# Kernel optimization log

Measured on AMD Instinct MI355X. Metric: run time of the kernel, lower is better.

The kernel has to match this reference:

```python
import jax, jax.numpy as jnp
import numpy as np

N = 10000      # miRNA_numbers (nodes)
E = 320000     # similarity-graph edges (avg degree 32)
M = 4          # modalities / channel_num (doc, role, tpcp, ernie)
D = 256        # per-modality feature dim (doc_dim=role_dim=tpcp_dim=ernie_dim)
P = 256        # pro_dim
NEG_SLOPE = 0.2  # PyG GATConv default negative_slope


def setup_inputs() -> dict:
    key = jax.random.key(0)
    ks = jax.random.split(key, 10)
    s = 1.0 / np.sqrt(D).astype(np.float32)
    return {
        "x_feats": jax.random.normal(ks[0], (M, N, D), jnp.float32),
        "edge_index": jax.random.randint(ks[1], (2, E), 0, N, dtype=jnp.int32),
        "Wg": jax.random.normal(ks[2], (M, D, D), jnp.float32) * s,      # GAT lin weights
        "a_src": jax.random.normal(ks[3], (M, D), jnp.float32) * s,      # GAT att_src
        "a_dst": jax.random.normal(ks[4], (M, D), jnp.float32) * s,      # GAT att_dst
        "bg": jnp.zeros((M, D), jnp.float32),                            # GAT bias
        "Wp": jax.random.normal(ks[5], (M, D, P), jnp.float32) * s,      # per-modality Linear(d, pro_dim)
        "bp": jnp.zeros((M, P), jnp.float32),
        "conv_w": jax.random.normal(ks[6], (M,), jnp.float32) * 0.5,     # 1x1 Conv2d channel mixer
        "conv_b": jnp.zeros((), jnp.float32),
    }


def reference(x_feats, edge_index, Wg, a_src, a_dst, bg, Wp, bp, conv_w, conv_b):
    n = x_feats.shape[1]
    loop = jnp.arange(n, dtype=edge_index.dtype)
    # PyG GATConv adds self-loops by default
    src = jnp.concatenate([edge_index[0], loop])  # [E+N]
    dst = jnp.concatenate([edge_index[1], loop])  # [E+N]

    def gat(x, W, asrc, adst, b):
        h = x @ W                                            # [N, D]
        alpha = (h * asrc).sum(-1)[src] + (h * adst).sum(-1)[dst]
        alpha = jax.nn.leaky_relu(alpha, NEG_SLOPE)          # [E+N]
        mx = jax.ops.segment_max(alpha, dst, num_segments=n)
        e = jnp.exp(alpha - mx[dst])
        denom = jax.ops.segment_sum(e, dst, num_segments=n) + 1e-16
        coef = e / denom[dst]                                # edge softmax per destination
        out = jax.ops.segment_sum(h[src] * coef[:, None], dst, num_segments=n)
        return out + b

    # 4 modality GATs over the same graph (eval mode: dropout = identity)
    h = jax.nn.relu(jax.vmap(gat)(x_feats, Wg, a_src, a_dst, bg))      # [M, N, D]
    xp = jnp.einsum('mnd,mdp->mnp', h, Wp) + bp[:, None, :]            # per-modality projection
    # 1x1 conv channel fusion across the M modality channels
    fused = jnp.einsum('m,mnp->np', conv_w, xp) + conv_b               # [N, P]
    return fused
```

## Files before the change

kernel.cpp:

```cpp
#include <hip/hip_runtime.h>
#include <hip/hip_bf16.h>
#include <cstdint>
#include <cstddef>

constexpr int kN = 10000;
constexpr int kE = 320000;
constexpr int kM = 4;
constexpr int kD = 256;
constexpr int kP = 256;
constexpr float kSlope = 0.2f;
constexpr int kCap = 96;

typedef __attribute__((ext_vector_type(8))) short bf16x8;
typedef __attribute__((ext_vector_type(4))) float f32x4;
typedef __attribute__((ext_vector_type(2))) float f32x2;

__device__ __forceinline__ unsigned short f2bf(float f) {
  union { float ff; unsigned int i; } v; v.ff = f;
  unsigned int x = v.i;
  unsigned int r = x + 0x7fffu + ((x >> 16) & 1u);
  return (unsigned short)(r >> 16);
}
__device__ __forceinline__ uint4 pack8(float4 a, float4 b) {
  uint4 o;
  o.x = (unsigned)f2bf(a.x) | ((unsigned)f2bf(a.y) << 16);
  o.y = (unsigned)f2bf(a.z) | ((unsigned)f2bf(a.w) << 16);
  o.z = (unsigned)f2bf(b.x) | ((unsigned)f2bf(b.y) << 16);
  o.w = (unsigned)f2bf(b.z) | ((unsigned)f2bf(b.w) << 16);
  return o;
}
__device__ __forceinline__ void gload_lds16(const void* g, void* l) {
  __builtin_amdgcn_global_load_lds((const __attribute__((address_space(1))) unsigned int*)g,
                                   (__attribute__((address_space(3))) unsigned int*)l, 16, 0, 0);
}


__global__ __launch_bounds__(256) void weight_prep_kernel(
    const float* __restrict__ Wg, const float* __restrict__ bp,
    const float* __restrict__ cw, const float* __restrict__ cb,
    unsigned short* __restrict__ Wgt, float* __restrict__ biasp, int* __restrict__ cnt) {
  const int blk = blockIdx.x;
  if (blk >= 65) {
    int z = blk - 65;
    int t = threadIdx.x;
    if (t < 250) ((int4*)cnt)[z * 250 + t] = make_int4(0, 0, 0, 0);
    return;
  }
  if (blk == 64) {
    int p = threadIdx.x;
    float v = cb[0];
#pragma unroll
    for (int mm = 0; mm < kM; mm++) v += cw[mm] * bp[mm * kP + p];
    biasp[p] = v;
    return;
  }
  __shared__ float tile[64][65];
  const int m = blk >> 4;
  const int t2 = blk & 15;
  const int r0 = (t2 >> 2) * 64;
  const int c0 = (t2 & 3) * 64;
  const float* in = Wg + ((size_t)m << 16);
#pragma unroll
  for (int l = 0; l < 16; l++) {
    int idx = l * 256 + threadIdx.x;
    int rr = idx >> 6, cc = idx & 63;
    tile[rr][cc] = in[(size_t)(c0 + rr) * 256 + r0 + cc];
  }
  __syncthreads();
#pragma unroll
  for (int l = 0; l < 16; l++) {
    int idx = l * 256 + threadIdx.x;
    int rr = idx >> 6, cc = idx & 63;
    Wgt[((size_t)m << 16) + (size_t)(r0 + rr) * 256 + c0 + cc] = f2bf(tile[cc][rr]);
  }
}


constexpr int ASTR = 64 * 8 + 8;
constexpr int BSTR = 256 * 8 + 8;
constexpr int kAsBytes = 2 * 4 * ASTR * 2;
constexpr int kBsBytes = 2 * 4 * BSTR * 2;

__global__ __launch_bounds__(256) void gemm_h_csr_mfma(
    const float* __restrict__ x, const unsigned short* __restrict__ Wgt,
    const float* __restrict__ asrc, const float* __restrict__ adst,
    const int* __restrict__ ei, int* __restrict__ cnt, int* __restrict__ csr_src,
    const float* __restrict__ Wp, const float* __restrict__ cw,
    unsigned short* __restrict__ Wqt,
    unsigned short* __restrict__ hb, float* __restrict__ sv, float* __restrict__ tv) {
  const int blk = blockIdx.x;
  const int tid = threadIdx.x;

  __shared__ __align__(16) char smem[kAsBytes + kBsBytes];
  __shared__ float sred[256], tred[256];
  auto As = (unsigned short(*)[4 * ASTR])smem;
  auto Bs = (unsigned short(*)[4 * BSTR])(smem + kAsBytes);

  if (blk >= 945) {
    auto tile = (float(*)[65])smem;
    const int b = blk - 945;
    const int m = b >> 4;
    const int t2 = b & 15;
    const int r0 = (t2 >> 2) * 64;
    const int c0 = (t2 & 3) * 64;
    const float* in = Wp + ((size_t)m << 16);
    const float scale = cw[m];
#pragma unroll
    for (int l = 0; l < 16; l++) {
      int idx = l * 256 + tid;
      int rr = idx >> 6, cc = idx & 63;
      tile[rr][cc] = in[(size_t)(c0 + rr) * 256 + r0 + cc] * scale;
    }
    __syncthreads();
#pragma unroll
    for (int l = 0; l < 16; l++) {
      int idx = l * 256 + tid;
      int rr = idx >> 6, cc = idx & 63;
      Wqt[(size_t)(r0 + rr) * 1024 + (m << 8) + c0 + cc] = f2bf(tile[cc][rr]);
    }
    return;
  }

  if (blk >= 632) {
    int t = (blk - 632) * 256 + tid;
    int e4 = t * 4;
    if (e4 >= kE) return;
    int4 s4 = *(const int4*)&ei[e4];
    int4 d4 = *(const int4*)&ei[kE + e4];
    int sl;
    sl = atomicAdd(&cnt[d4.x], 1); csr_src[d4.x * kCap + sl] = s4.x;
    sl = atomicAdd(&cnt[d4.y], 1); csr_src[d4.y * kCap + sl] = s4.y;
    sl = atomicAdd(&cnt[d4.z], 1); csr_src[d4.z * kCap + sl] = s4.z;
    sl = atomicAdd(&cnt[d4.w], 1); csr_src[d4.w * kCap + sl] = s4.w;
    return;
  }

  const int m = (blk & 7) >> 1;
  const int i = (blk >> 3) * 2 + (blk & 1);
  if (i >= 157) return;
  const int row0 = i * 64;

  const int wave = tid >> 6, lane = tid & 63;
  const int lidx = lane & 15, lslot = lane >> 4;
  const int wcol0 = wave * 64;

  const int arow_s = tid & 63, aslot_s = tid >> 6;
  const int agr = min(row0 + arow_s, kN - 1);
  const float* Abase = x + ((size_t)m * kN + agr) * kD + aslot_s * 8;
  const unsigned short* Bbase = Wgt + (size_t)m * kD * kD;

  f32x4 acc[4][4] = {};

  {
    float4 f0 = *(const float4*)(Abase);
    float4 f1 = *(const float4*)(Abase + 4);
    *(uint4*)&As[0][aslot_s * ASTR + arow_s * 8] = pack8(f0, f1);
#pragma unroll
    for (int l = 0; l < 4; l++) {
      int c = tid + l * 256;
      int col = c & 255, slot = c >> 8;
      gload_lds16(Bbase + (size_t)col * kD + slot * 8, &Bs[0][slot * BSTR + col * 8]);
    }
  }
  __syncthreads();

  int buf = 0;
  for (int t = 0; t < 8; t++) {
    float4 f0, f1;
    const bool pf = (t < 7);
    if (pf) {
      const int k1 = (t + 1) * 32;
      f0 = *(const float4*)(Abase + k1);
      f1 = *(const float4*)(Abase + k1 + 4);
#pragma unroll
      for (int l = 0; l < 4; l++) {
        int c = tid + l * 256;
        int col = c & 255, slot = c >> 8;
        gload_lds16(Bbase + (size_t)col * kD + k1 + slot * 8,
                    &Bs[buf ^ 1][slot * BSTR + col * 8]);
      }
    }
    bf16x8 a[4], bfr[4];
#pragma unroll
    for (int i2 = 0; i2 < 4; i2++)
      a[i2] = *(const bf16x8*)&As[buf][lslot * ASTR + (i2 * 16 + lidx) * 8];
#pragma unroll
    for (int j = 0; j < 4; j++)
      bfr[j] = *(const bf16x8*)&Bs[buf][lslot * BSTR + (wcol0 + j * 16 + lidx) * 8];
#pragma unroll
    for (int i2 = 0; i2 < 4; i2++)
#pragma unroll
      for (int j = 0; j < 4; j++)
        acc[i2][j] = __builtin_amdgcn_mfma_f32_16x16x32_bf16(a[i2], bfr[j], acc[i2][j], 0, 0, 0);
    if (pf) {
      *(uint4*)&As[buf ^ 1][aslot_s * ASTR + arow_s * 8] = pack8(f0, f1);
    }
    __syncthreads();
    buf ^= 1;
  }

  const int slot4 = lane >> 4;
  float av[4], dv[4];
#pragma unroll
  for (int j = 0; j < 4; j++) {
    av[j] = asrc[m * kD + wcol0 + j * 16 + lidx];
    dv[j] = adst[m * kD + wcol0 + j * 16 + lidx];
  }
#pragma unroll
  for (int i2 = 0; i2 < 4; i2++) {
#pragma unroll
    for (int reg = 0; reg < 4; reg++) {
      int grow = row0 + i2 * 16 + slot4 * 4 + reg;
      float sp = 0.f, tp = 0.f;
#pragma unroll
      for (int j = 0; j < 4; j++) {
        float hv = acc[i2][j][reg];
        sp += hv * av[j];
        tp += hv * dv[j];
        if (grow < kN) hb[((size_t)m * kN + grow) * kD + wcol0 + j * 16 + lidx] = f2bf(hv);
      }
#pragma unroll
      for (int o = 1; o < 16; o <<= 1) {
        sp += __shfl_xor(sp, o);
        tp += __shfl_xor(tp, o);
      }
      if (lidx == 0) {
        sred[wave * 64 + i2 * 16 + slot4 * 4 + reg] = sp;
        tred[wave * 64 + i2 * 16 + slot4 * 4 + reg] = tp;
      }
    }
  }
  __syncthreads();
  if (tid < 64) {
    int grow = row0 + tid;
    if (grow < kN) {
      float s = sred[tid] + sred[64 + tid] + sred[128 + tid] + sred[192 + tid];
      float t = tred[tid] + tred[64 + tid] + tred[128 + tid] + tred[192 + tid];
      sv[m * kN + grow] = s;
      tv[m * kN + grow] = t;
    }
  }
}


__global__ __launch_bounds__(512) void gat_aggregate_kernel(
    const unsigned short* __restrict__ hb, const float* __restrict__ sv,
    const float* __restrict__ tv, const float* __restrict__ bg,
    const int* __restrict__ cnt, const int* __restrict__ csr_src,
    unsigned short* __restrict__ hrelb) {
  const int l = blockIdx.x;
  const int xcd = l & 7;
  const int m = xcd >> 1;
  const int ngroup = (l >> 3) * 2 + (xcd & 1);
  const int n = ngroup * 8 + (threadIdx.x >> 6);
  const int lane = threadIdx.x & 63;
  const int half = lane >> 5;
  const int lf = lane & 31;
  const int fb = lf * 8;

  const float tt = tv[m * kN + n];
  const int b = n * kCap;
  const int deg = cnt[n];

  float a_self = sv[m * kN + n] + tt;
  a_self = fmaxf(a_self, kSlope * a_self);
  const float e_self = __expf(a_self);

  const unsigned short* hm = hb + ((size_t)m * kN << 8) + fb;
  f32x2 acc2[4] = {};
  {
    const float es = half ? 0.f : e_self;
    const f32x2 es2 = {es, es};
    uint4 hx = *(const uint4*)(hm + ((size_t)n << 8));
#pragma unroll
    for (int q = 0; q < 4; q++) {
      unsigned w = ((const unsigned*)&hx)[q];
      f32x2 hv2 = {__uint_as_float(w << 16), __uint_as_float(w & 0xffff0000u)};
      acc2[q] = __builtin_elementwise_fma(hv2, es2, acc2[q]);
    }
  }
  float denom = (lane == 0) ? e_self : 0.f;

  for (int c0 = 0; c0 < deg; c0 += 64) {
    int j = c0 + lane;
    float ee = 0.f;
    int src = 0;
    if (j < deg) {
      src = csr_src[b + j];
      float a = sv[m * kN + src] + tt;
      a = fmaxf(a, kSlope * a);
      ee = __expf(a);
    }
    denom += ee;
    const int cl = min(64, deg - c0);
    for (int j2 = 0; j2 < cl; j2 += 8) {
#pragma unroll
      for (int p = 0; p < 4; p++) {
        int ja = j2 + 2 * p;
        float ep = __shfl(ee, ja + half);
        int sp = __shfl(src, ja + half);
        uint4 hx = *(const uint4*)(hm + ((size_t)sp << 8));
        const f32x2 ep2 = {ep, ep};
#pragma unroll
        for (int q = 0; q < 4; q++) {
          unsigned w = ((const unsigned*)&hx)[q];
          f32x2 hv2 = {__uint_as_float(w << 16), __uint_as_float(w & 0xffff0000u)};
          acc2[q] = __builtin_elementwise_fma(hv2, ep2, acc2[q]);
        }
      }
    }
  }
#pragma unroll
  for (int o = 32; o > 0; o >>= 1) denom += __shfl_xor(denom, o);
  const float inv = 1.f / (denom + 1e-16f);

#pragma unroll
  for (int q = 0; q < 4; q++) {
    acc2[q].x += __shfl_xor(acc2[q].x, 32);
    acc2[q].y += __shfl_xor(acc2[q].y, 32);
  }

  if (half == 0) {
    const float* bgp = bg + m * kD + fb;
    float4 b0 = *(const float4*)bgp;
    float4 b1 = *(const float4*)(bgp + 4);
    float4 o0, o1;
    o0.x = fmaxf(acc2[0].x * inv + b0.x, 0.f);
    o0.y = fmaxf(acc2[0].y * inv + b0.y, 0.f);
    o0.z = fmaxf(acc2[1].x * inv + b0.z, 0.f);
    o0.w = fmaxf(acc2[1].y * inv + b0.w, 0.f);
    o1.x = fmaxf(acc2[2].x * inv + b1.x, 0.f);
    o1.y = fmaxf(acc2[2].y * inv + b1.y, 0.f);
    o1.z = fmaxf(acc2[3].x * inv + b1.z, 0.f);
    o1.w = fmaxf(acc2[3].y * inv + b1.w, 0.f);
    *(uint4*)(hrelb + (((size_t)m * kN + n) << 8) + fb) = pack8(o0, o1);
  }
}


constexpr int FSTR = 64 * 8 + 8;

__global__ __launch_bounds__(256) void gemm_fused_mfma(const unsigned short* __restrict__ hrelb,
                                                       const unsigned short* __restrict__ Wqt,
                                                       const float* __restrict__ biasp,
                                                       float* __restrict__ out) {
  const int l = blockIdx.x;
  const int xcd = l & 7;
  const int t0 = l >> 3;
  const int c = t0 & 3;
  const int r = (t0 >> 2) * 8 + xcd;
  if (r >= 157) return;
  const int row0 = r * 64;
  const int col0 = c * 64;

  const int tid = threadIdx.x;
  const int wave = tid >> 6, lane = tid & 63;
  const int lidx = lane & 15, lslot = lane >> 4;
  const int wr = wave >> 1, wc = wave & 1;

  __shared__ __align__(16) unsigned short As[2][8 * FSTR];
  __shared__ __align__(16) unsigned short Bs[2][8 * FSTR];

  f32x4 acc[2][2] = {};

  const int arow = min(row0 + (tid & 63), kN - 1);
  const int bcol = col0 + (tid & 63);

#pragma unroll
  for (int ll = 0; ll < 2; ll++) {
    int slot = (tid >> 6) + ll * 4;
    gload_lds16(hrelb + ((size_t)arow << 8) + slot * 8,
                &As[0][slot * FSTR + (tid & 63) * 8]);
    gload_lds16(Wqt + (size_t)bcol * 1024 + slot * 8,
                &Bs[0][slot * FSTR + (tid & 63) * 8]);
  }
  __syncthreads();

  int buf = 0;
  for (int t = 0; t < 16; t++) {
    if (t < 15) {
      const int k1 = (t + 1) * 64;
      const int mm = k1 >> 8;
      const int d1 = k1 & 255;
#pragma unroll
      for (int ll = 0; ll < 2; ll++) {
        int slot = (tid >> 6) + ll * 4;
        gload_lds16(hrelb + (((size_t)mm * kN + arow) << 8) + d1 + slot * 8,
                    &As[buf ^ 1][slot * FSTR + (tid & 63) * 8]);
        gload_lds16(Wqt + (size_t)bcol * 1024 + k1 + slot * 8,
                    &Bs[buf ^ 1][slot * FSTR + (tid & 63) * 8]);
      }
    }
#pragma unroll
    for (int s = 0; s < 2; s++) {
      const int ks = s * 4 + lslot;
      bf16x8 a[2], bfr[2];
#pragma unroll
      for (int i = 0; i < 2; i++)
        a[i] = *(const bf16x8*)&As[buf][ks * FSTR + (wr * 32 + i * 16 + lidx) * 8];
#pragma unroll
      for (int j = 0; j < 2; j++)
        bfr[j] = *(const bf16x8*)&Bs[buf][ks * FSTR + (wc * 32 + j * 16 + lidx) * 8];
#pragma unroll
      for (int i = 0; i < 2; i++)
#pragma unroll
        for (int j = 0; j < 2; j++)
          acc[i][j] = __builtin_amdgcn_mfma_f32_16x16x32_bf16(a[i], bfr[j], acc[i][j], 0, 0, 0);
    }
    __syncthreads();
    buf ^= 1;
  }

  const int slot4 = lane >> 4;
#pragma unroll
  for (int i = 0; i < 2; i++) {
#pragma unroll
    for (int reg = 0; reg < 4; reg++) {
      int grow = row0 + wr * 32 + i * 16 + slot4 * 4 + reg;
      if (grow < kN) {
#pragma unroll
        for (int j = 0; j < 2; j++) {
          int gcol = col0 + wc * 32 + j * 16 + lidx;
          out[(size_t)grow * kP + gcol] = acc[i][j][reg] + biasp[gcol];
        }
      }
    }
  }
}


extern "C" void kernel_launch(void* const* d_in, const int* in_sizes, int n_in,
                              void* d_out, int out_size, void* d_ws, size_t ws_size,
                              hipStream_t stream) {
  const float* x = (const float*)d_in[0];
  const int* ei = (const int*)d_in[1];
  const float* Wg = (const float*)d_in[2];
  const float* asrc = (const float*)d_in[3];
  const float* adst = (const float*)d_in[4];
  const float* bg = (const float*)d_in[5];
  const float* Wp = (const float*)d_in[6];
  const float* bp = (const float*)d_in[7];
  const float* cw = (const float*)d_in[8];
  const float* cb = (const float*)d_in[9];
  float* out = (float*)d_out;

  char* ws = (char*)d_ws;
  size_t off = 0;
  auto alloc = [&](size_t bytes) -> void* {
    void* p = ws + off;
    off = (off + bytes + 255) & ~(size_t)255;
    return p;
  };
  unsigned short* hb = (unsigned short*)alloc((size_t)kM * kN * kD * 2);
  unsigned short* hrelb = (unsigned short*)alloc((size_t)kM * kN * kD * 2);
  unsigned short* Wgt = (unsigned short*)alloc((size_t)kM * kD * kD * 2);
  unsigned short* Wqt = (unsigned short*)alloc((size_t)kP * kM * kD * 2);
  float* sv = (float*)alloc((size_t)kM * kN * sizeof(float));
  float* tv = (float*)alloc((size_t)kM * kN * sizeof(float));
  float* biasp = (float*)alloc(kP * sizeof(float));
  int* cnt = (int*)alloc(kN * sizeof(int));
  int* csr_src = (int*)alloc((size_t)kN * kCap * sizeof(int));

  weight_prep_kernel<<<75, 256, 0, stream>>>(Wg, bp, cw, cb, Wgt, biasp, cnt);

  gemm_h_csr_mfma<<<1009, 256, 0, stream>>>(x, Wgt, asrc, adst, ei, cnt, csr_src,
                                            Wp, cw, Wqt, hb, sv, tv);

  gat_aggregate_kernel<<<5000, 512, 0, stream>>>(hb, sv, tv, bg, cnt, csr_src, hrelb);

  gemm_fused_mfma<<<640, 256, 0, stream>>>(hrelb, Wqt, biasp, out);
}
```

Baseline: 118.0 us.

## Split per-modality features into two 128-wide halves for L2-local gather

Stores h and the relu'd aggregate in a [M*2][N][128] layout, splitting each 256-wide feature row into two halves. Each XCD (selected from the block index) now handles one modality-half, so its gather working set is half as large and more of it can stay in that XCD's L2. The aggregate kernel uses 256-thread blocks of 4 nodes, with each wave processing 4 neighbors at a time over 16 lanes, and the grid grows to 20000 blocks. The cost is more blocks, an extra cross-lane reduction step, and the attention scalars being recomputed for each half.

```diff
diff --git a/kernel.cpp b/kernel.cpp
--- a/kernel.cpp
+++ b/kernel.cpp
@@ -10,6 +10,7 @@
 constexpr int kP = 256;
 constexpr float kSlope = 0.2f;
 constexpr int kCap = 96;
+
 
 typedef __attribute__((ext_vector_type(8))) short bf16x8;
 typedef __attribute__((ext_vector_type(4))) float f32x4;
@@ -217,7 +218,10 @@
         float hv = acc[i2][j][reg];
         sp += hv * av[j];
         tp += hv * dv[j];
-        if (grow < kN) hb[((size_t)m * kN + grow) * kD + wcol0 + j * 16 + lidx] = f2bf(hv);
+        if (grow < kN) {
+          int gcol = wcol0 + j * 16 + lidx;
+          hb[(((size_t)(m * 2) + (gcol >> 7)) * kN + grow) * 128 + (gcol & 127)] = f2bf(hv);
+        }
       }
 #pragma unroll
       for (int o = 1; o < 16; o <<= 1) {
@@ -243,7 +247,7 @@
 }
 
 
-__global__ __launch_bounds__(512) void gat_aggregate_kernel(
+__global__ __launch_bounds__(256) void gat_aggregate_kernel(
     const unsigned short* __restrict__ hb, const float* __restrict__ sv,
     const float* __restrict__ tv, const float* __restrict__ bg,
     const int* __restrict__ cnt, const int* __restrict__ csr_src,
@@ -251,11 +255,12 @@
   const int l = blockIdx.x;
   const int xcd = l & 7;
   const int m = xcd >> 1;
-  const int ngroup = (l >> 3) * 2 + (xcd & 1);
-  const int n = ngroup * 8 + (threadIdx.x >> 6);
+  const int h = xcd & 1;
+  const int ngroup = l >> 3;
+  const int n = ngroup * 4 + (threadIdx.x >> 6);
   const int lane = threadIdx.x & 63;
-  const int half = lane >> 5;
-  const int lf = lane & 31;
+  const int q = lane >> 4;
+  const int lf = lane & 15;
   const int fb = lf * 8;
 
   const float tt = tv[m * kN + n];
@@ -266,17 +271,17 @@
   a_self = fmaxf(a_self, kSlope * a_self);
   const float e_self = __expf(a_self);
 
-  const unsigned short* hm = hb + ((size_t)m * kN << 8) + fb;
+  const unsigned short* hm = hb + ((((size_t)m * 2 + h) * kN) << 7) + fb;
   f32x2 acc2[4] = {};
   {
-    const float es = half ? 0.f : e_self;
+    const float es = (q == 0) ? e_self : 0.f;
     const f32x2 es2 = {es, es};
-    uint4 hx = *(const uint4*)(hm + ((size_t)n << 8));
-#pragma unroll
-    for (int q = 0; q < 4; q++) {
-      unsigned w = ((const unsigned*)&hx)[q];
+    uint4 hx = *(const uint4*)(hm + ((size_t)n << 7));
+#pragma unroll
+    for (int k = 0; k < 4; k++) {
+      unsigned w = ((const unsigned*)&hx)[k];
       f32x2 hv2 = {__uint_as_float(w << 16), __uint_as_float(w & 0xffff0000u)};
-      acc2[q] = __builtin_elementwise_fma(hv2, es2, acc2[q]);
+      acc2[k] = __builtin_elementwise_fma(hv2, es2, acc2[k]);
     }
   }
   float denom = (lane == 0) ? e_self : 0.f;
@@ -293,20 +298,17 @@
     }
     denom += ee;
     const int cl = min(64, deg - c0);
-    for (int j2 = 0; j2 < cl; j2 += 8) {
-#pragma unroll
-      for (int p = 0; p < 4; p++) {
-        int ja = j2 + 2 * p;
-        float ep = __shfl(ee, ja + half);
-        int sp = __shfl(src, ja + half);
-        uint4 hx = *(const uint4*)(hm + ((size_t)sp << 8));
-        const f32x2 ep2 = {ep, ep};
-#pragma unroll
-        for (int q = 0; q < 4; q++) {
-          unsigned w = ((const unsigned*)&hx)[q];
-          f32x2 hv2 = {__uint_as_float(w << 16), __uint_as_float(w & 0xffff0000u)};
-          acc2[q] = __builtin_elementwise_fma(hv2, ep2, acc2[q]);
-        }
+    for (int j2 = 0; j2 < cl; j2 += 4) {
+      int ja = j2 + q;
+      float ep = __shfl(ee, ja);
+      int sp = __shfl(src, ja);
+      uint4 hx = *(const uint4*)(hm + ((size_t)sp << 7));
+      const f32x2 ep2 = {ep, ep};
+#pragma unroll
+      for (int k = 0; k < 4; k++) {
+        unsigned w = ((const unsigned*)&hx)[k];
+        f32x2 hv2 = {__uint_as_float(w << 16), __uint_as_float(w & 0xffff0000u)};
+        acc2[k] = __builtin_elementwise_fma(hv2, ep2, acc2[k]);
       }
     }
   }
@@ -315,13 +317,15 @@
   const float inv = 1.f / (denom + 1e-16f);
 
 #pragma unroll
-  for (int q = 0; q < 4; q++) {
-    acc2[q].x += __shfl_xor(acc2[q].x, 32);
-    acc2[q].y += __shfl_xor(acc2[q].y, 32);
-  }
-
-  if (half == 0) {
-    const float* bgp = bg + m * kD + fb;
+  for (int k = 0; k < 4; k++) {
+    acc2[k].x += __shfl_xor(acc2[k].x, 16);
+    acc2[k].y += __shfl_xor(acc2[k].y, 16);
+    acc2[k].x += __shfl_xor(acc2[k].x, 32);
+    acc2[k].y += __shfl_xor(acc2[k].y, 32);
+  }
+
+  if (lane < 16) {
+    const float* bgp = bg + m * kD + h * 128 + fb;
     float4 b0 = *(const float4*)bgp;
     float4 b1 = *(const float4*)(bgp + 4);
     float4 o0, o1;
@@ -333,7 +337,7 @@
     o1.y = fmaxf(acc2[2].y * inv + b1.y, 0.f);
     o1.z = fmaxf(acc2[3].x * inv + b1.z, 0.f);
     o1.w = fmaxf(acc2[3].y * inv + b1.w, 0.f);
-    *(uint4*)(hrelb + (((size_t)m * kN + n) << 8) + fb) = pack8(o0, o1);
+    *(uint4*)(hrelb + ((((size_t)m * 2 + h) * kN + n) << 7) + fb) = pack8(o0, o1);
   }
 }
 
@@ -366,11 +370,18 @@
   const int arow = min(row0 + (tid & 63), kN - 1);
   const int bcol = col0 + (tid & 63);
 
+  auto a_src = [&](int k1, int slot) -> const unsigned short* {
+    const int mm = k1 >> 8;
+    const int d1 = k1 & 255;
+    const int hf = d1 >> 7;
+    const int dd = d1 & 127;
+    return hrelb + ((((size_t)mm * 2 + hf) * kN + arow) << 7) + dd + slot * 8;
+  };
+
 #pragma unroll
   for (int ll = 0; ll < 2; ll++) {
     int slot = (tid >> 6) + ll * 4;
-    gload_lds16(hrelb + ((size_t)arow << 8) + slot * 8,
-                &As[0][slot * FSTR + (tid & 63) * 8]);
+    gload_lds16(a_src(0, slot), &As[0][slot * FSTR + (tid & 63) * 8]);
     gload_lds16(Wqt + (size_t)bcol * 1024 + slot * 8,
                 &Bs[0][slot * FSTR + (tid & 63) * 8]);
   }
@@ -380,13 +391,10 @@
   for (int t = 0; t < 16; t++) {
     if (t < 15) {
       const int k1 = (t + 1) * 64;
-      const int mm = k1 >> 8;
-      const int d1 = k1 & 255;
 #pragma unroll
       for (int ll = 0; ll < 2; ll++) {
         int slot = (tid >> 6) + ll * 4;
-        gload_lds16(hrelb + (((size_t)mm * kN + arow) << 8) + d1 + slot * 8,
-                    &As[buf ^ 1][slot * FSTR + (tid & 63) * 8]);
+        gload_lds16(a_src(k1, slot), &As[buf ^ 1][slot * FSTR + (tid & 63) * 8]);
         gload_lds16(Wqt + (size_t)bcol * 1024 + k1 + slot * 8,
                     &Bs[buf ^ 1][slot * FSTR + (tid & 63) * 8]);
       }
@@ -466,7 +474,7 @@
   gemm_h_csr_mfma<<<1009, 256, 0, stream>>>(x, Wgt, asrc, adst, ei, cnt, csr_src,
                                             Wp, cw, Wqt, hb, sv, tv);
 
-  gat_aggregate_kernel<<<5000, 512, 0, stream>>>(hb, sv, tv, bg, cnt, csr_src, hrelb);
+  gat_aggregate_kernel<<<20000, 256, 0, stream>>>(hb, sv, tv, bg, cnt, csr_src, hrelb);
 
   gemm_fused_mfma<<<640, 256, 0, stream>>>(hrelb, Wqt, biasp, out);
 }
```

After: 126.5 us. 1.07x slower.

## Load GEMM B fragments directly from global and shrink aggregate blocks

Applied to the files above, without the earlier changes.

Both MFMA GEMMs stop staging the bf16 weight operand through LDS. Each wave now reads its B fragments straight from global memory (L2-resident weights), which cuts LDS footprint, LDS traffic and the matching async copies. The cost is more global/L2 load latency inside the inner loop with no prefetch. Separately, the GAT aggregation kernel moves from 512-thread blocks of 8 nodes to 256-thread blocks of 4 nodes, doubling the grid, which changes occupancy and scheduling granularity.

```diff
diff --git a/kernel.cpp b/kernel.cpp
--- a/kernel.cpp
+++ b/kernel.cpp
@@ -77,9 +77,8 @@
 
 
 constexpr int ASTR = 64 * 8 + 8;
-constexpr int BSTR = 256 * 8 + 8;
 constexpr int kAsBytes = 2 * 4 * ASTR * 2;
-constexpr int kBsBytes = 2 * 4 * BSTR * 2;
+constexpr int kSmemBytes = 64 * 65 * 4;
 
 __global__ __launch_bounds__(256) void gemm_h_csr_mfma(
     const float* __restrict__ x, const unsigned short* __restrict__ Wgt,
@@ -91,10 +90,9 @@
   const int blk = blockIdx.x;
   const int tid = threadIdx.x;
 
-  __shared__ __align__(16) char smem[kAsBytes + kBsBytes];
+  __shared__ __align__(16) char smem[kSmemBytes];
   __shared__ float sred[256], tred[256];
   auto As = (unsigned short(*)[4 * ASTR])smem;
-  auto Bs = (unsigned short(*)[4 * BSTR])(smem + kAsBytes);
 
   if (blk >= 945) {
     auto tile = (float(*)[65])smem;
@@ -147,7 +145,7 @@
   const int arow_s = tid & 63, aslot_s = tid >> 6;
   const int agr = min(row0 + arow_s, kN - 1);
   const float* Abase = x + ((size_t)m * kN + agr) * kD + aslot_s * 8;
-  const unsigned short* Bbase = Wgt + (size_t)m * kD * kD;
+  const unsigned short* Bcol = Wgt + (size_t)m * kD * kD + (size_t)(wcol0 + lidx) * kD + lslot * 8;
 
   f32x4 acc[4][4] = {};
 
@@ -155,38 +153,26 @@
     float4 f0 = *(const float4*)(Abase);
     float4 f1 = *(const float4*)(Abase + 4);
     *(uint4*)&As[0][aslot_s * ASTR + arow_s * 8] = pack8(f0, f1);
-#pragma unroll
-    for (int l = 0; l < 4; l++) {
-      int c = tid + l * 256;
-      int col = c & 255, slot = c >> 8;
-      gload_lds16(Bbase + (size_t)col * kD + slot * 8, &Bs[0][slot * BSTR + col * 8]);
-    }
   }
   __syncthreads();
 
   int buf = 0;
   for (int t = 0; t < 8; t++) {
+    const int k0 = t * 32;
     float4 f0, f1;
     const bool pf = (t < 7);
     if (pf) {
-      const int k1 = (t + 1) * 32;
-      f0 = *(const float4*)(Abase + k1);
-      f1 = *(const float4*)(Abase + k1 + 4);
-#pragma unroll
-      for (int l = 0; l < 4; l++) {
-        int c = tid + l * 256;
-        int col = c & 255, slot = c >> 8;
-        gload_lds16(Bbase + (size_t)col * kD + k1 + slot * 8,
-                    &Bs[buf ^ 1][slot * BSTR + col * 8]);
-      }
-    }
-    bf16x8 a[4], bfr[4];
+      f0 = *(const float4*)(Abase + k0 + 32);
+      f1 = *(const float4*)(Abase + k0 + 36);
+    }
+    bf16x8 bfr[4];
+#pragma unroll
+    for (int j = 0; j < 4; j++)
+      bfr[j] = *(const bf16x8*)(Bcol + (size_t)(j * 16) * kD + k0);
+    bf16x8 a[4];
 #pragma unroll
     for (int i2 = 0; i2 < 4; i2++)
       a[i2] = *(const bf16x8*)&As[buf][lslot * ASTR + (i2 * 16 + lidx) * 8];
-#pragma unroll
-    for (int j = 0; j < 4; j++)
-      bfr[j] = *(const bf16x8*)&Bs[buf][lslot * BSTR + (wcol0 + j * 16 + lidx) * 8];
 #pragma unroll
     for (int i2 = 0; i2 < 4; i2++)
 #pragma unroll
@@ -243,7 +229,7 @@
 }
 
 
-__global__ __launch_bounds__(512) void gat_aggregate_kernel(
+__global__ __launch_bounds__(256) void gat_aggregate_kernel(
     const unsigned short* __restrict__ hb, const float* __restrict__ sv,
     const float* __restrict__ tv, const float* __restrict__ bg,
     const int* __restrict__ cnt, const int* __restrict__ csr_src,
@@ -252,7 +238,7 @@
   const int xcd = l & 7;
   const int m = xcd >> 1;
   const int ngroup = (l >> 3) * 2 + (xcd & 1);
-  const int n = ngroup * 8 + (threadIdx.x >> 6);
+  const int n = ngroup * 4 + (threadIdx.x >> 6);
   const int lane = threadIdx.x & 63;
   const int half = lane >> 5;
   const int lf = lane & 31;
@@ -359,27 +345,25 @@
   const int wr = wave >> 1, wc = wave & 1;
 
   __shared__ __align__(16) unsigned short As[2][8 * FSTR];
-  __shared__ __align__(16) unsigned short Bs[2][8 * FSTR];
 
   f32x4 acc[2][2] = {};
 
   const int arow = min(row0 + (tid & 63), kN - 1);
-  const int bcol = col0 + (tid & 63);
+  const unsigned short* Bcol = Wqt + (size_t)(col0 + wc * 32 + lidx) * 1024;
 
 #pragma unroll
   for (int ll = 0; ll < 2; ll++) {
     int slot = (tid >> 6) + ll * 4;
     gload_lds16(hrelb + ((size_t)arow << 8) + slot * 8,
                 &As[0][slot * FSTR + (tid & 63) * 8]);
-    gload_lds16(Wqt + (size_t)bcol * 1024 + slot * 8,
-                &Bs[0][slot * FSTR + (tid & 63) * 8]);
   }
   __syncthreads();
 
   int buf = 0;
   for (int t = 0; t < 16; t++) {
+    const int k0 = t * 64;
     if (t < 15) {
-      const int k1 = (t + 1) * 64;
+      const int k1 = k0 + 64;
       const int mm = k1 >> 8;
       const int d1 = k1 & 255;
 #pragma unroll
@@ -387,8 +371,6 @@
         int slot = (tid >> 6) + ll * 4;
         gload_lds16(hrelb + (((size_t)mm * kN + arow) << 8) + d1 + slot * 8,
                     &As[buf ^ 1][slot * FSTR + (tid & 63) * 8]);
-        gload_lds16(Wqt + (size_t)bcol * 1024 + k1 + slot * 8,
-                    &Bs[buf ^ 1][slot * FSTR + (tid & 63) * 8]);
       }
     }
 #pragma unroll
@@ -400,7 +382,7 @@
         a[i] = *(const bf16x8*)&As[buf][ks * FSTR + (wr * 32 + i * 16 + lidx) * 8];
 #pragma unroll
       for (int j = 0; j < 2; j++)
-        bfr[j] = *(const bf16x8*)&Bs[buf][ks * FSTR + (wc * 32 + j * 16 + lidx) * 8];
+        bfr[j] = *(const bf16x8*)(Bcol + (size_t)(j * 16) * 1024 + k0 + ks * 8);
 #pragma unroll
       for (int i = 0; i < 2; i++)
 #pragma unroll
@@ -466,7 +448,7 @@
   gemm_h_csr_mfma<<<1009, 256, 0, stream>>>(x, Wgt, asrc, adst, ei, cnt, csr_src,
                                             Wp, cw, Wqt, hb, sv, tv);
 
-  gat_aggregate_kernel<<<5000, 512, 0, stream>>>(hb, sv, tv, bg, cnt, csr_src, hrelb);
+  gat_aggregate_kernel<<<kN, 256, 0, stream>>>(hb, sv, tv, bg, cnt, csr_src, hrelb);
 
   gemm_fused_mfma<<<640, 256, 0, stream>>>(hrelb, Wqt, biasp, out);
 }
```

Result: slower. 122.1 us (+3.5%).
